# Kernel optimization log

Measured on AMD Instinct MI355X. Metric: run time of the kernel, lower is better.

The kernel has to match this reference:

```python
import jax, jax.numpy as jnp
import numpy as np


def setup_inputs() -> dict:
    key = jax.random.key(0)
    B, T, H, W = 32, 1024, 32, 32
    dim_s = 32
    # spike ids per (batch, time, h, w), values in [0, dim_s)
    inp = jax.random.randint(key, (B, T, H, W), 0, dim_s, dtype=jnp.int32)
    return {"input": inp, "dim_s": dim_s}


def reference(input, dim_s):
    # input: [B, T, H, W] int32 spike ids in [0, dim_s)
    # out:   [B, dim_s, H, W] int32 counts: out[b,s,h,w] = #{t : input[b,t,h,w]==s}
    B, T, H, W = input.shape
    b_idx = jnp.arange(B, dtype=jnp.int32)[:, None, None, None]   # [B,1,1,1]
    h_idx = jnp.arange(H, dtype=jnp.int32)[None, None, :, None]   # [1,1,H,1]
    w_idx = jnp.arange(W, dtype=jnp.int32)[None, None, None, :]   # [1,1,1,W]
    hist = jnp.zeros((B, dim_s, H, W), dtype=jnp.int32)
    # scatter-add one count per (b, t, h, w) into bin input[b,t,h,w]
    hist = hist.at[b_idx, input, h_idx, w_idx].add(jnp.int32(1))
    return hist
```

## Files before the change

### kernel.cpp

```cpp
#include <hip/hip_runtime.h>


constexpr int T_DIM   = 1024;
constexpr int HW      = 1024;
constexpr int DIM_S   = 32;
constexpr int PIX_PB  = 64;
constexpr int TQ      = 8;
constexpr int THREADS = PIX_PB * TQ;
constexpr int T_PER_THREAD = T_DIM / TQ;
constexpr int PLANE_CHUNKS = HW / PIX_PB;

__global__ __launch_bounds__(THREADS) void spike_hist_kernel(
    const int* __restrict__ in, int* __restrict__ out) {
    __shared__ int lds_w[8][THREADS];

    const int tid  = threadIdx.x;
    const int blk  = blockIdx.x;
    const int b    = blk >> 4;
    const int pix0 = (blk & (PLANE_CHUNKS - 1)) * PIX_PB;
    const int pix  = tid & (PIX_PB - 1);
    const int tq   = tid >> 6;

    const int* __restrict__ p = in
        + (size_t)b * (T_DIM * HW)
        + (size_t)(tq * T_PER_THREAD) * HW
        + pix0 + pix;

    unsigned w[8] = {0u, 0u, 0u, 0u, 0u, 0u, 0u, 0u};

    #pragma unroll 8
    for (int i = 0; i < T_PER_THREAD; ++i) {
        const int v = p[(size_t)i * HW];
        const unsigned inc = 1u << ((v & 3) << 3);
        const int sel = v >> 2;
        #pragma unroll
        for (int j = 0; j < 8; ++j)
            w[j] += (sel == j) ? inc : 0u;
    }

    #pragma unroll
    for (int j = 0; j < 8; ++j) lds_w[j][tid] = (int)w[j];
    __syncthreads();

    int* __restrict__ outb = out + (size_t)b * (DIM_S * HW) + pix0;
    #pragma unroll
    for (int r = 0; r < 4; ++r) {
        const int e    = r * THREADS + tid;
        const int opix = e & (PIX_PB - 1);
        const int s    = e >> 6;
        const int word = s >> 2;
        const int sh   = (s & 3) << 3;
        int sum = 0;
        #pragma unroll
        for (int q = 0; q < TQ; ++q)
            sum += (int)(((unsigned)lds_w[word][q * PIX_PB + opix] >> sh) & 0xFFu);
        outb[(size_t)s * HW + opix] = sum;
    }
}

extern "C" void kernel_launch(void* const* d_in, const int* in_sizes, int n_in,
                              void* d_out, int out_size, void* d_ws, size_t ws_size,
                              hipStream_t stream) {
    const int* in = (const int*)d_in[0];
    int* out      = (int*)d_out;
    const int B   = in_sizes[0] / (T_DIM * HW);
    const int grid = B * PLANE_CHUNKS;
    spike_hist_kernel<<<grid, THREADS, 0, stream>>>(in, out);
}
```

Before: 193.6 us.

## Replace packed-byte counters with bit-sliced popcount histogram per 32 timesteps

After: 194.6 us. About the same (+0.5%).

```diff
diff --git a/kernel.cpp b/kernel.cpp
--- a/kernel.cpp
+++ b/kernel.cpp
@@ -9,10 +9,11 @@
 constexpr int THREADS = PIX_PB * TQ;
 constexpr int T_PER_THREAD = T_DIM / TQ;
 constexpr int PLANE_CHUNKS = HW / PIX_PB;
+constexpr int NGROUP  = T_PER_THREAD / 32;
 
 __global__ __launch_bounds__(THREADS) void spike_hist_kernel(
     const int* __restrict__ in, int* __restrict__ out) {
-    __shared__ int lds_w[8][THREADS];
+    __shared__ int lds[DIM_S][THREADS];
 
     const int tid  = threadIdx.x;
     const int blk  = blockIdx.x;
@@ -26,20 +27,46 @@
         + (size_t)(tq * T_PER_THREAD) * HW
         + pix0 + pix;
 
-    unsigned w[8] = {0u, 0u, 0u, 0u, 0u, 0u, 0u, 0u};
+    int cnt[DIM_S];
+    #pragma unroll
+    for (int s = 0; s < DIM_S; ++s) cnt[s] = 0;
 
-    #pragma unroll 8
-    for (int i = 0; i < T_PER_THREAD; ++i) {
-        const int v = p[(size_t)i * HW];
-        const unsigned inc = 1u << ((v & 3) << 3);
-        const int sel = v >> 2;
+    #pragma unroll
+    for (int g = 0; g < NGROUP; ++g) {
+        unsigned p0 = 0, p1 = 0, p2 = 0, p3 = 0, p4 = 0;
         #pragma unroll
-        for (int j = 0; j < 8; ++j)
-            w[j] += (sel == j) ? inc : 0u;
+        for (int h = 0; h < 2; ++h) {
+            unsigned v[16];
+            #pragma unroll
+            for (int i = 0; i < 16; ++i)
+                v[i] = (unsigned)p[(size_t)(g * 32 + h * 16 + i) * HW];
+            #pragma unroll
+            for (int i = 0; i < 16; ++i) {
+                const int sh = h * 16 + i;
+                const unsigned x = v[i];
+                p0 |= (x        & 1u) << sh;
+                p1 |= ((x >> 1) & 1u) << sh;
+                p2 |= ((x >> 2) & 1u) << sh;
+                p3 |= ((x >> 3) & 1u) << sh;
+                p4 |= ((x >> 4) & 1u) << sh;
+            }
+        }
+        const unsigned n0 = ~p0, n1 = ~p1, n2 = ~p2, n3 = ~p3, n4 = ~p4;
+        const unsigned a[4]  = { n1 & n0, n1 & p0, p1 & n0, p1 & p0 };
+        const unsigned bq[4] = { n3 & n2, n3 & p2, p3 & n2, p3 & p2 };
+        #pragma unroll
+        for (int j = 0; j < 4; ++j) {
+            #pragma unroll
+            for (int k = 0; k < 4; ++k) {
+                const unsigned ab = bq[j] & a[k];
+                cnt[j * 4 + k]      += __builtin_popcount(ab & n4);
+                cnt[16 + j * 4 + k] += __builtin_popcount(ab & p4);
+            }
+        }
     }
 
     #pragma unroll
-    for (int j = 0; j < 8; ++j) lds_w[j][tid] = (int)w[j];
+    for (int s = 0; s < DIM_S; ++s) lds[s][tid] = cnt[s];
     __syncthreads();
 
     int* __restrict__ outb = out + (size_t)b * (DIM_S * HW) + pix0;
@@ -48,12 +75,10 @@
         const int e    = r * THREADS + tid;
         const int opix = e & (PIX_PB - 1);
         const int s    = e >> 6;
-        const int word = s >> 2;
-        const int sh   = (s & 3) << 3;
         int sum = 0;
         #pragma unroll
         for (int q = 0; q < TQ; ++q)
-            sum += (int)(((unsigned)lds_w[word][q * PIX_PB + opix] >> sh) & 0xFFu);
+            sum += lds[s][q * PIX_PB + opix];
         outb[(size_t)s * HW + opix] = sum;
     }
 }
```
